# Kernel tuning notes

Hardware: AMD Instinct MI355X
Metric: run time of the kernel (lower is better)

Reference implementation:

```python
import jax, jax.numpy as jnp
import numpy as np

EPROJS = 512
ODIM = 600
DLAYERS = 2
DUNITS = 512
EMBED_DIM = 512
JOINT_DIM = 512
BLANK = 0


def setup_inputs() -> dict:
    key = jax.random.key(0)
    ks = jax.random.split(key, 20)
    B, T, U = 16, 200, 64
    s_d = 1.0 / np.sqrt(DUNITS)
    s_e = 1.0 / np.sqrt(EPROJS)
    s_j = 1.0 / np.sqrt(JOINT_DIM)
    inp = {
        "hs_pad": jax.random.normal(ks[0], (B, T, EPROJS), dtype=jnp.float32),
        "ys_in_pad": jax.random.randint(ks[1], (B, U), 0, ODIM),
        "embed_table": jax.random.normal(ks[2], (ODIM, EMBED_DIM), dtype=jnp.float32).at[BLANK].set(0.0),
        # LSTMCell layer 0: input EMBED_DIM -> DUNITS (gates i,f,g,o stacked => 4*DUNITS)
        "W_ih0": jax.random.uniform(ks[3], (4 * DUNITS, EMBED_DIM), minval=-s_d, maxval=s_d),
        "W_hh0": jax.random.uniform(ks[4], (4 * DUNITS, DUNITS), minval=-s_d, maxval=s_d),
        "b_ih0": jax.random.uniform(ks[5], (4 * DUNITS,), minval=-s_d, maxval=s_d),
        "b_hh0": jax.random.uniform(ks[6], (4 * DUNITS,), minval=-s_d, maxval=s_d),
        # LSTMCell layer 1: DUNITS -> DUNITS
        "W_ih1": jax.random.uniform(ks[7], (4 * DUNITS, DUNITS), minval=-s_d, maxval=s_d),
        "W_hh1": jax.random.uniform(ks[8], (4 * DUNITS, DUNITS), minval=-s_d, maxval=s_d),
        "b_ih1": jax.random.uniform(ks[9], (4 * DUNITS,), minval=-s_d, maxval=s_d),
        "b_hh1": jax.random.uniform(ks[10], (4 * DUNITS,), minval=-s_d, maxval=s_d),
        # joint network
        "W_enc": jax.random.uniform(ks[11], (JOINT_DIM, EPROJS), minval=-s_e, maxval=s_e),
        "b_enc": jax.random.uniform(ks[12], (JOINT_DIM,), minval=-s_e, maxval=s_e),
        "W_dec": jax.random.uniform(ks[13], (JOINT_DIM, DUNITS), minval=-s_d, maxval=s_d),
        "W_out": jax.random.uniform(ks[14], (ODIM, JOINT_DIM), minval=-s_j, maxval=s_j),
        "b_out": jax.random.uniform(ks[15], (ODIM,), minval=-s_j, maxval=s_j),
    }
    return inp


def _lstm_cell(x, h, c, W_ih, W_hh, b_ih, b_hh):
    gates = x @ W_ih.T + b_ih + h @ W_hh.T + b_hh  # (B, 4*D)
    i, f, g, o = jnp.split(gates, 4, axis=-1)
    c_new = jax.nn.sigmoid(f) * c + jax.nn.sigmoid(i) * jnp.tanh(g)
    h_new = jax.nn.sigmoid(o) * jnp.tanh(c_new)
    return h_new, c_new


def _decode(eys, W_ih0, W_hh0, b_ih0, b_hh0, W_ih1, W_hh1, b_ih1, b_hh1):
    # eys: (B, U, E). Sequential 2-layer LSTM over U via scan.
    B = eys.shape[0]
    z = jnp.zeros((B, DUNITS), dtype=eys.dtype)
    carry0 = (z, z, z, z)  # h0, c0, h1, c1

    def step(carry, ey):
        h0, c0, h1, c1 = carry
        h0, c0 = _lstm_cell(ey, h0, c0, W_ih0, W_hh0, b_ih0, b_hh0)
        h1, c1 = _lstm_cell(h0, h1, c1, W_ih1, W_hh1, b_ih1, b_hh1)
        return (h0, c0, h1, c1), h1

    _, h_dec = jax.lax.scan(step, carry0, jnp.swapaxes(eys, 0, 1))  # (U, B, D)
    return jnp.swapaxes(h_dec, 0, 1)  # (B, U, D)


def reference(hs_pad, ys_in_pad, embed_table, W_ih0, W_hh0, b_ih0, b_hh0,
              W_ih1, W_hh1, b_ih1, b_hh1, W_enc, b_enc, W_dec, W_out, b_out):
    eys = embed_table[ys_in_pad]  # (B, U, E); dropout = identity at p=0
    h_dec = _decode(eys, W_ih0, W_hh0, b_ih0, b_hh0, W_ih1, W_hh1, b_ih1, b_hh1)
    # Joint: project BEFORE broadcasting (thin GEMMs), then broadcast-add.
    enc_p = hs_pad @ W_enc.T + b_enc            # (B, T, J)
    dec_p = h_dec @ W_dec.T                     # (B, U, J)
    z = jnp.tanh(enc_p[:, :, None, :] + dec_p[:, None, :, :])  # (B, T, U, J)
    return z @ W_out.T + b_out                  # (B, T, U, odim)
```

## Files before the change

kernel.cpp:

```cpp
#include <hip/hip_runtime.h>
#include <hip/hip_bf16.h>
#include <stdint.h>

#define DEVI __device__ __forceinline__

typedef unsigned short u16;
typedef __attribute__((ext_vector_type(8))) short short8;
typedef __attribute__((ext_vector_type(4))) float f32x4;
typedef __attribute__((ext_vector_type(16))) float f32x16;

DEVI u16 f2bf(float f) {
  union { float f; uint32_t u; } v; v.f = f;
  return (u16)((v.u + 0x7fffu + ((v.u >> 16) & 1u)) >> 16);
}
DEVI float tanh_c(float x) {
  float e = __expf(x + x);
  float r = __builtin_amdgcn_rcpf(e + 1.0f);
  return __builtin_fmaf(-2.0f, r, 1.0f);
}
DEVI float sigm(float x) { return __builtin_amdgcn_rcpf(1.0f + __expf(-x)); }
DEVI uint32_t tj2(float a, float b) {
  float ea = __expf(a + a), eb = __expf(b + b);
  float ta = __builtin_fmaf(-2.0f, __builtin_amdgcn_rcpf(ea + 1.0f), 1.0f);
  float tb = __builtin_fmaf(-2.0f, __builtin_amdgcn_rcpf(eb + 1.0f), 1.0f);
  union { __hip_bfloat162 h; uint32_t u; } cv;
  cv.h = __float22bfloat162_rn(make_float2(ta, tb));
  return cv.u;
}
DEVI short8 ald16(const u16* p) {
  union { unsigned long long q[2]; short8 v; } u;
  u.q[0] = __hip_atomic_load((unsigned long long*)p,       __ATOMIC_RELAXED, __HIP_MEMORY_SCOPE_AGENT);
  u.q[1] = __hip_atomic_load((unsigned long long*)(p + 4), __ATOMIC_RELAXED, __HIP_MEMORY_SCOPE_AGENT);
  return u.v;
}

__global__ void prep_kernel(
    const float* __restrict__ W_ih0, const float* __restrict__ W_hh0,
    const float* __restrict__ W_ih1, const float* __restrict__ W_hh1,
    const float* __restrict__ W_enc, const float* __restrict__ W_dec,
    const float* __restrict__ W_out, const float* __restrict__ embed,
    const float* __restrict__ hs_pad,
    const float* __restrict__ b_ih0, const float* __restrict__ b_hh0,
    const float* __restrict__ b_ih1, const float* __restrict__ b_hh1,
    const float* __restrict__ b_out,
    u16* __restrict__ Wih0b, u16* __restrict__ Whh0b,
    u16* __restrict__ Wih1b, u16* __restrict__ Whh1b,
    u16* __restrict__ Wencb, u16* __restrict__ Wdecb,
    u16* __restrict__ embedb, u16* __restrict__ hsb,
    u16* __restrict__ Wshufb,
    float* __restrict__ bsum0, float* __restrict__ bsum1, float* __restrict__ boutp)
{
  const int c1 = 1048576, c2 = 2097152, c3 = 3145728, c4 = 4194304;
  const int c5 = 4456448, c6 = 4718592, c7 = 5025792, c8 = 6664192;
  const int c9 = 6991872, c10 = 6993920, c11 = 6995968, c12 = 6996608;
  for (int i = blockIdx.x * blockDim.x + threadIdx.x; i < c12; i += gridDim.x * blockDim.x) {
    if (i < c1)       Wih0b[i]      = f2bf(W_ih0[i]);
    else if (i < c2)  Whh0b[i - c1] = f2bf(W_hh0[i - c1]);
    else if (i < c3)  Wih1b[i - c2] = f2bf(W_ih1[i - c2]);
    else if (i < c4)  Whh1b[i - c3] = f2bf(W_hh1[i - c3]);
    else if (i < c5)  Wencb[i - c4] = f2bf(W_enc[i - c4]);
    else if (i < c6)  Wdecb[i - c5] = f2bf(W_dec[i - c5]);
    else if (i < c7)  embedb[i - c6] = f2bf(embed[i - c6]);
    else if (i < c8)  hsb[i - c7]   = f2bf(hs_pad[i - c7]);
    else if (i < c9) {
      int e = i - c8;
      int kc = e / 10240, r = e % 10240;
      int tile = r >> 9, r2 = r & 511;
      int lane = r2 >> 3, ii = r2 & 7;
      int n = tile * 32 + (lane & 31);
      int k = kc * 16 + ((lane >> 5) << 3) + ii;
      Wshufb[e] = (n < 600) ? f2bf(W_out[n * 512 + k]) : (u16)0;
    }
    else if (i < c10) { int n = i - c9;  bsum0[n] = b_ih0[n] + b_hh0[n]; }
    else if (i < c11) { int n = i - c10; bsum1[n] = b_ih1[n] + b_hh1[n]; }
    else              { int n = i - c11; boutp[n] = (n < 600) ? b_out[n] : 0.0f; }
  }
}

template<int MODE, bool AAT, bool SAT>
DEVI void gemm_tile(const u16* __restrict__ A, const u16* __restrict__ B,
                    const int* __restrict__ ys, const float* __restrict__ bias,
                    float* __restrict__ out, int N, int m0, int n0, int tid)
{
  int wv = tid >> 6, l = tid & 63;
  int row = m0 + wv * 16 + (l & 15);
  const u16* arow;
  if (MODE == 1) { int uu = row >> 4, bb = row & 15; arow = A + (size_t)ys[bb * 64 + uu] * 512; }
  else           arow = A + (size_t)row * 512;
  int kof = (l >> 4) * 8;
  arow += kof;
  const u16* br = B + (size_t)(n0 + (l & 15)) * 512 + kof;
  f32x4 a0 = {0.f,0.f,0.f,0.f}, a1 = a0, a2 = a0, a3 = a0;
  for (int kk = 0; kk < 512; kk += 32) {
    short8 av = AAT ? ald16(arow + kk) : *(const short8*)(arow + kk);
    short8 b0 = *(const short8*)(br + kk);
    short8 b1 = *(const short8*)(br + 8192 + kk);
    short8 b2 = *(const short8*)(br + 16384 + kk);
    short8 b3 = *(const short8*)(br + 24576 + kk);
    a0 = __builtin_amdgcn_mfma_f32_16x16x32_bf16(av, b0, a0, 0, 0, 0);
    a1 = __builtin_amdgcn_mfma_f32_16x16x32_bf16(av, b1, a1, 0, 0, 0);
    a2 = __builtin_amdgcn_mfma_f32_16x16x32_bf16(av, b2, a2, 0, 0, 0);
    a3 = __builtin_amdgcn_mfma_f32_16x16x32_bf16(av, b3, a3, 0, 0, 0);
  }
  int col = l & 15, rb = m0 + wv * 16 + (l >> 4) * 4;
  f32x4 accs[4] = {a0, a1, a2, a3};
#pragma unroll
  for (int g = 0; g < 4; ++g) {
    int n = n0 + g * 16 + col;
    float bs = bias ? bias[n] : 0.0f;
#pragma unroll
    for (int i2 = 0; i2 < 4; ++i2) {
      float v = accs[g][i2] + bs;
      if (SAT)
        __hip_atomic_store(&out[(size_t)(rb + i2) * N + n], v,
                           __ATOMIC_RELAXED, __HIP_MEMORY_SCOPE_AGENT);
      else
        out[(size_t)(rb + i2) * N + n] = v;
    }
  }
}

#define L0WG 32
#define FUSED_WG 1136

DEVI void waitflags(const int* f0, const int* f1, const int* xc, int n0, int n1, int xneed) {
  if (threadIdx.x < 64) {
    int l = threadIdx.x;
    for (;;) {
      int a = __hip_atomic_load((int*)(f0 + (l & 31) * 16), __ATOMIC_RELAXED, __HIP_MEMORY_SCOPE_AGENT);
      int b = __hip_atomic_load((int*)(f1 + l * 16),        __ATOMIC_RELAXED, __HIP_MEMORY_SCOPE_AGENT);
      int c = xc ? __hip_atomic_load((int*)xc, __ATOMIC_RELAXED, __HIP_MEMORY_SCOPE_AGENT) : xneed;
      if (__all(a >= n0 && b >= n1 && c >= xneed)) break;
      __builtin_amdgcn_s_sleep(1);
    }
    __builtin_amdgcn_fence(__ATOMIC_ACQUIRE, "agent");
  }
  __syncthreads();
}
DEVI void postflag(int* slot, int val) {
  __syncthreads();
  if (threadIdx.x == 0)
    __hip_atomic_store(slot, val, __ATOMIC_RELAXED, __HIP_MEMORY_SCOPE_AGENT);
}
DEVI const u16* haddr(const u16* base, int slot, int k, int b) {
  return base + slot * 8192 + (k >> 4) * 256 + b * 16 + (k & 15);
}
DEVI void hstore(u16* base, int idx, u16 mine, int tid) {
  int other = __shfl_xor((int)mine, 1);
  if (!(tid & 1)) {
    uint32_t pkv = (uint32_t)mine | (((uint32_t)other & 0xffffu) << 16);
    __hip_atomic_store((uint32_t*)(base + idx), pkv, __ATOMIC_RELAXED, __HIP_MEMORY_SCOPE_AGENT);
  }
}

__global__ __launch_bounds__(256) void lstm_fused(
    const u16* __restrict__ embedb, const u16* __restrict__ Wih0b,
    const int* __restrict__ ys, const float* __restrict__ bsum0,
    float* __restrict__ Xg0,
    const u16* __restrict__ hsb, const u16* __restrict__ Wencb,
    const float* __restrict__ b_enc, float* __restrict__ enc_p,
    const u16* __restrict__ Wdecb, float* __restrict__ dec_p,
    const u16* __restrict__ Whh0, const u16* __restrict__ Wih1, const u16* __restrict__ Whh1,
    const float* __restrict__ bsum1,
    u16* __restrict__ h0b, u16* __restrict__ h1b,
    u16* __restrict__ Hdec,
    int* __restrict__ flags0, int* __restrict__ flags1, int* __restrict__ xcnt)
{
  __shared__ float red[16][256];
  const int bid = blockIdx.x, tid = threadIdx.x;
  const int wv = tid >> 6, l = tid & 63;
  const int lb = l & 15, kof = (l >> 4) * 8;
  const int drb = (l >> 4) * 4;

  if (bid >= 96) {
    if (bid < 608) {
      int g = bid - 96, mt = g >> 5, nt = g & 31;
      gemm_tile<1, false, true>(embedb, Wih0b, ys, bsum0, Xg0, 2048,
                                mt * 64, nt * 64, tid);
      asm volatile("s_waitcnt vmcnt(0)" ::: "memory");
      __syncthreads();
      if (tid == 0)
        __hip_atomic_fetch_add(xcnt + mt, 1, __ATOMIC_RELAXED, __HIP_MEMORY_SCOPE_AGENT);
    } else if (bid < 1008) {
      int g = bid - 608, mt = g >> 3, nt = g & 7;
      gemm_tile<0, false, false>(hsb, Wencb, nullptr, b_enc, enc_p, 512,
                                 mt * 64, nt * 64, tid);
    } else {
      int g = bid - 1008, mt = g >> 3, nt = g & 7;
      const int need = mt * 4 + 4;
      if (tid < 64) {
        for (;;) {
          int a = __hip_atomic_load((int*)(flags1 + tid * 16), __ATOMIC_RELAXED, __HIP_MEMORY_SCOPE_AGENT);
          if (__all(a >= need)) break;
          __builtin_amdgcn_s_sleep(8);
        }
        __builtin_amdgcn_fence(__ATOMIC_ACQUIRE, "agent");
      }
      __syncthreads();
      gemm_tile<0, true, false>(Hdec, Wdecb, nullptr, nullptr, dec_p, 512,
                                mt * 64, nt * 64, tid);
    }
    return;
  }

  if (bid < L0WG) {
    const int be = tid >> 4, je = tid & 15, jg = (bid << 4) + je;
    short8 breg[16];
#pragma unroll
    for (int g = 0; g < 4; ++g) {
      const u16* bp = Whh0 + (size_t)(g * 512 + bid * 16 + lb) * 512 + wv * 128 + kof;
#pragma unroll
      for (int ks = 0; ks < 4; ++ks)
        breg[g * 4 + ks] = *(const short8*)(bp + ks * 32);
    }
    float c0 = 0.f;
    for (int t = 0; t < 64; ++t) {
      waitflags(flags0, flags1, xcnt + (t >> 2), t, (t > 7) ? (t - 7) : 0, 32);
      const float* xg = Xg0 + (size_t)((t << 4) + be) * 2048 + jg;
      float x0 = __hip_atomic_load((float*)(xg),        __ATOMIC_RELAXED, __HIP_MEMORY_SCOPE_AGENT);
      float x1 = __hip_atomic_load((float*)(xg + 512),  __ATOMIC_RELAXED, __HIP_MEMORY_SCOPE_AGENT);
      float x2 = __hip_atomic_load((float*)(xg + 1024), __ATOMIC_RELAXED, __HIP_MEMORY_SCOPE_AGENT);
      float x3 = __hip_atomic_load((float*)(xg + 1536), __ATOMIC_RELAXED, __HIP_MEMORY_SCOPE_AGENT);
      const int rs = (t + 7) & 7;
      f32x4 g0 = {0.f,0.f,0.f,0.f}, g1 = g0, g2 = g0, g3 = g0;
#pragma unroll
      for (int ks = 0; ks < 4; ++ks) {
        int kk = wv * 128 + ks * 32 + kof;
        short8 av = ald16(haddr(h0b, rs, kk, lb));
        g0 = __builtin_amdgcn_mfma_f32_16x16x32_bf16(av, breg[0 * 4 + ks], g0, 0, 0, 0);
        g1 = __builtin_amdgcn_mfma_f32_16x16x32_bf16(av, breg[1 * 4 + ks], g1, 0, 0, 0);
        g2 = __builtin_amdgcn_mfma_f32_16x16x32_bf16(av, breg[2 * 4 + ks], g2, 0, 0, 0);
        g3 = __builtin_amdgcn_mfma_f32_16x16x32_bf16(av, breg[3 * 4 + ks], g3, 0, 0, 0);
      }
      f32x4 gs[4] = {g0, g1, g2, g3};
#pragma unroll
      for (int g = 0; g < 4; ++g)
#pragma unroll
        for (int i2 = 0; i2 < 4; ++i2)
          red[wv * 4 + g][(drb + i2) * 16 + lb] = gs[g][i2];
      __syncthreads();
      {
        float s0 = 0, s1 = 0, s2 = 0, s3 = 0;
#pragma unroll
        for (int v2 = 0; v2 < 4; ++v2) {
          s0 += red[v2 * 4 + 0][be * 16 + je]; s1 += red[v2 * 4 + 1][be * 16 + je];
          s2 += red[v2 * 4 + 2][be * 16 + je]; s3 += red[v2 * 4 + 3][be * 16 + je];
        }
        float gi = s0 + x0, gf = s1 + x1, gg = s2 + x2, go = s3 + x3;
        float I = sigm(gi), F = sigm(gf), G = tanh_c(gg), O = sigm(go);
        c0 = F * c0 + I * G;
        float h0 = O * tanh_c(c0);
        hstore(h0b, ((t & 7) * 32 + bid) * 256 + (tid & ~1), f2bf(h0), tid);
      }
      postflag(flags0 + bid * 16, t + 1);
    }
  } else {
    const int v = bid - L0WG;
    const u16* base0 = (wv < 2) ? Wih1 : Whh1;
    const int kbase = (wv & 1) * 256;
    short8 breg[16];
#pragma unroll
    for (int tt = 0; tt < 2; ++tt) {
      int c = tt * 16 + lb, gate = c >> 3, du = c & 7;
      const u16* bp = base0 + (size_t)(gate * 512 + v * 8 + du) * 512 + kbase + kof;
#pragma unroll
      for (int ks = 0; ks < 8; ++ks)
        breg[tt * 8 + ks] = *(const short8*)(bp + ks * 32);
    }
    float bs0 = 0, bs1 = 0, bs2 = 0, bs3 = 0, c1 = 0.f;
    if (tid < 128) {
      int du = tid & 7, ju = v * 8 + du;
      bs0 = bsum1[ju]; bs1 = bsum1[512 + ju]; bs2 = bsum1[1024 + ju]; bs3 = bsum1[1536 + ju];
    }
    for (int t = 0; t < 64; ++t) {
      waitflags(flags0, flags1, nullptr, t + 1, t, 0);
      const u16* hsrc = (wv < 2) ? (h0b + (t & 7) * 8192) : (h1b + ((t + 7) & 7) * 8192);
      f32x4 g0 = {0.f,0.f,0.f,0.f}, g1 = g0;
#pragma unroll
      for (int ks = 0; ks < 8; ++ks) {
        int kk = kbase + ks * 32 + kof;
        short8 av = ald16(hsrc + (kk >> 4) * 256 + lb * 16 + (kk & 15));
        g0 = __builtin_amdgcn_mfma_f32_16x16x32_bf16(av, breg[0 * 8 + ks], g0, 0, 0, 0);
        g1 = __builtin_amdgcn_mfma_f32_16x16x32_bf16(av, breg[1 * 8 + ks], g1, 0, 0, 0);
      }
#pragma unroll
      for (int i2 = 0; i2 < 4; ++i2) {
        red[wv * 2 + 0][(drb + i2) * 16 + lb] = g0[i2];
        red[wv * 2 + 1][(drb + i2) * 16 + lb] = g1[i2];
      }
      __syncthreads();
      if (tid < 128) {
        int be = tid >> 3, du = tid & 7, ju = v * 8 + du;
        float sg[4] = {bs0, bs1, bs2, bs3};
#pragma unroll
        for (int g = 0; g < 4; ++g) {
          int c = g * 8 + du, tt = c >> 4, cc = c & 15;
          float acc = 0.f;
#pragma unroll
          for (int w2 = 0; w2 < 4; ++w2) acc += red[w2 * 2 + tt][be * 16 + cc];
          sg[g] += acc;
        }
        float I = sigm(sg[0]), F = sigm(sg[1]), G = tanh_c(sg[2]), O = sigm(sg[3]);
        c1 = F * c1 + I * G;
        float h1v = O * tanh_c(c1);
        u16 hb = f2bf(h1v);
        int idx = ((t & 7) * 32 + (ju >> 4)) * 256 + be * 16 + (ju & 15);
        hstore(h1b, idx & ~1, hb, tid);
        hstore(Hdec, ((t << 4) + be) * 512 + (ju & ~1), hb, tid);
      }
      postflag(flags1 + v * 16, t + 1);
    }
  }
}

__global__ __launch_bounds__(256) void joint_kernel(
    const float* __restrict__ enc_p,
    const float* __restrict__ dec_p,
    const u16* __restrict__ Wshuf,
    const float* __restrict__ boutp,
    float* __restrict__ out)
{
  __shared__ int4 wlds[2][1280];
  __shared__ int4 zlds[2][256];
  int bid = blockIdx.x;
  int b = bid / 400, rem = bid % 400;
  int tb = rem / 8, rem2 = rem % 8;
  int ub = rem2 >> 1, nh = rem2 & 1;
  int tid = threadIdx.x, wv = tid >> 6, l = tid & 63;
  int mv = wv >> 1, nv = wv & 1;
  int ln31 = l & 31, lh = l >> 5;
  const int tile0 = nv * 5;
  f32x16 acc[5];
#pragma unroll
  for (int j = 0; j < 5; ++j) {
    float bv = boutp[nh * 320 + (tile0 + j) * 32 + ln31];
#pragma unroll
    for (int g = 0; g < 16; ++g) acc[j][g] = bv;
  }
  int zr = tid & 63, zg = tid >> 6;
  const float* er = enc_p + (size_t)(b * 200 + tb * 4 + (zr >> 4)) * 512 + zg * 8;
  const float* dr = dec_p + (size_t)((ub * 16 + (zr & 15)) * 16 + b) * 512 + zg * 8;
  const int zslot = ((zg >> 1) * 2 + (zr >> 5)) * 64 + ((zg & 1) << 5) + (zr & 31);
  const int4* gW = (const int4*)Wshuf;
  const int nhof = nh * 640;
  const int L0 = tid, L1 = 256 + tid, L2 = 512 + tid + ((tid >= 128) ? 640 : 0),
            L3 = 1408 + tid, L4 = 1664 + tid;
  const int S2 = 512 + tid;

  int4 aw0, aw1, aw2, aw3, aw4; float4 ae0, ae1, ad0, ad1;
  int4 bw0, bw1, bw2, bw3, bw4; float4 be0, be1, bd0, bd1;

  {
    int4 w0 = gW[nhof + L0], w1 = gW[nhof + L1], w2 = gW[nhof + L2],
         w3 = gW[nhof + L3], w4 = gW[nhof + L4];
    float4 e0 = *(const float4*)(er),     e1 = *(const float4*)(er + 4);
    float4 d0 = *(const float4*)(dr),     d1 = *(const float4*)(dr + 4);
    const int cb1 = 2560 + nhof;
    aw0 = gW[cb1 + L0]; aw1 = gW[cb1 + L1]; aw2 = gW[cb1 + L2];
    aw3 = gW[cb1 + L3]; aw4 = gW[cb1 + L4];
    ae0 = *(const float4*)(er + 32); ae1 = *(const float4*)(er + 36);
    ad0 = *(const float4*)(dr + 32); ad1 = *(const float4*)(dr + 36);
    int4 pk;
    pk.x = (int)tj2(e0.x + d0.x, e0.y + d0.y);
    pk.y = (int)tj2(e0.z + d0.z, e0.w + d0.w);
    pk.z = (int)tj2(e1.x + d1.x, e1.y + d1.y);
    pk.w = (int)tj2(e1.z + d1.z, e1.w + d1.w);
    zlds[0][zslot] = pk;
    wlds[0][tid] = w0; wlds[0][256 + tid] = w1; wlds[0][S2] = w2;
    wlds[0][768 + tid] = w3; wlds[0][1024 + tid] = w4;
    __syncthreads();
  }

#define JBODY(C, CUR, NXT, W0, W1, W2, W3, W4, E0, E1, D0, D1,                  \
              PW0, PW1, PW2, PW3, PW4, PE0, PE1, PD0, PD1)                      \
  {                                                                             \
    if ((C) + 2 <= 15) {                                                        \
      const int cb = ((C) + 2) * 2560 + nhof;                                   \
      PW0 = gW[cb + L0]; PW1 = gW[cb + L1]; PW2 = gW[cb + L2];                  \
      PW3 = gW[cb + L3]; PW4 = gW[cb + L4];                                     \
      int k0 = ((C) + 2) * 32;                                                  \
      PE0 = *(const float4*)(er + k0); PE1 = *(const float4*)(er + k0 + 4);     \
      PD0 = *(const float4*)(dr + k0); PD1 = *(const float4*)(dr + k0 + 4);     \
    }                                                                           \
    _Pragma("unroll")                                                           \
    for (int ks = 0; ks < 2; ++ks) {                                            \
      short8 aA = *(const short8*)&zlds[CUR][(ks * 2 + mv) * 64 + l];           \
      _Pragma("unroll")                                                         \
      for (int j = 0; j < 5; ++j) {                                             \
        short8 bw = *(const short8*)&wlds[CUR][ks * 640 + (tile0 + j) * 64 + l];\
        acc[j] = __builtin_amdgcn_mfma_f32_32x32x16_bf16(aA, bw, acc[j], 0, 0, 0); \
      }                                                                         \
    }                                                                           \
    if ((C) + 1 <= 15) {                                                        \
      wlds[NXT][tid] = W0; wlds[NXT][256 + tid] = W1; wlds[NXT][S2] = W2;       \
      wlds[NXT][768 + tid] = W3; wlds[NXT][1024 + tid] = W4;                    \
      int4 pk;                                                                  \
      pk.x = (int)tj2(E0.x + D0.x, E0.y + D0.y);                                \
      pk.y = (int)tj2(E0.z + D0.z, E0.w + D0.w);                                \
      pk.z = (int)tj2(E1.x + D1.x, E1.y + D1.y);                                \
      pk.w = (int)tj2(E1.z + D1.z, E1.w + D1.w);                                \
      zlds[NXT][zslot] = pk;                                                    \
    }                                                                           \
    __syncthreads();                                                            \
  }

  for (int cc = 0; cc < 8; ++cc) {
    const int c0 = cc * 2;
    JBODY(c0,     0, 1, aw0, aw1, aw2, aw3, aw4, ae0, ae1, ad0, ad1,
                        bw0, bw1, bw2, bw3, bw4, be0, be1, bd0, bd1);
    JBODY(c0 + 1, 1, 0, bw0, bw1, bw2, bw3, bw4, be0, be1, bd0, bd1,
                        aw0, aw1, aw2, aw3, aw4, ae0, ae1, ad0, ad1);
  }
#undef JBODY

#pragma unroll
  for (int j = 0; j < 5; ++j) {
    int n = nh * 320 + (tile0 + j) * 32 + ln31;
    if (n < 600) {
      int rbase = mv * 32 + 4 * lh;
#pragma unroll
      for (int g = 0; g < 16; ++g) {
        int r = rbase + (g & 3) + ((g >> 2) << 3);
        int tt = tb * 4 + (r >> 4), uu = ub * 16 + (r & 15);
        __builtin_nontemporal_store(
            acc[j][g], &out[(size_t)((b * 200 + tt) * 64 + uu) * 600 + n]);
      }
    }
  }
}

extern "C" void kernel_launch(void* const* d_in, const int* in_sizes, int n_in,
                              void* d_out, int out_size, void* d_ws, size_t ws_size,
                              hipStream_t stream) {
  const float* hs_pad = (const float*)d_in[0];
  const int*   ys     = (const int*)d_in[1];
  const float* embed  = (const float*)d_in[2];
  const float* W_ih0  = (const float*)d_in[3];
  const float* W_hh0  = (const float*)d_in[4];
  const float* b_ih0  = (const float*)d_in[5];
  const float* b_hh0  = (const float*)d_in[6];
  const float* W_ih1  = (const float*)d_in[7];
  const float* W_hh1  = (const float*)d_in[8];
  const float* b_ih1  = (const float*)d_in[9];
  const float* b_hh1  = (const float*)d_in[10];
  const float* W_enc  = (const float*)d_in[11];
  const float* b_enc  = (const float*)d_in[12];
  const float* W_dec  = (const float*)d_in[13];
  const float* W_out  = (const float*)d_in[14];
  const float* b_out  = (const float*)d_in[15];
  float* out = (float*)d_out;

  uint8_t* ws = (uint8_t*)d_ws;
  size_t off = 0;
  auto alloc = [&](size_t bytes) -> void* {
    void* p = ws + off;
    off = (off + bytes + 255) & ~(size_t)255;
    return p;
  };
  int* flags0   = (int*)alloc(2048);
  int* flags1   = (int*)alloc(4096);
  int* xcnt     = (int*)alloc(256);
  u16* h0buf    = (u16*)alloc(8 * 32 * 256 * 2);
  u16* h1buf    = (u16*)alloc(8 * 32 * 256 * 2);
  u16* Hdec     = (u16*)alloc(64 * 16 * 512 * 2);
  float* Xg0    = (float*)alloc(1024 * 2048 * 4);
  float* enc_p  = (float*)alloc(3200 * 512 * 4);
  float* dec_p  = (float*)alloc(1024 * 512 * 4);
  u16* Wih0b    = (u16*)alloc(2048 * 512 * 2);
  u16* Whh0b    = (u16*)alloc(2048 * 512 * 2);
  u16* Wih1b    = (u16*)alloc(2048 * 512 * 2);
  u16* Whh1b    = (u16*)alloc(2048 * 512 * 2);
  u16* Wencb    = (u16*)alloc(512 * 512 * 2);
  u16* Wdecb    = (u16*)alloc(512 * 512 * 2);
  u16* embedb   = (u16*)alloc(600 * 512 * 2);
  u16* hsb      = (u16*)alloc(3200 * 512 * 2);
  u16* Wshufb   = (u16*)alloc(32 * 20 * 64 * 8 * 2);
  float* bsum0  = (float*)alloc(2048 * 4);
  float* bsum1  = (float*)alloc(2048 * 4);
  float* boutp  = (float*)alloc(640 * 4);

  (void)hipMemsetAsync(d_ws, 0, 2048 + 4096 + 256 + 131072 + 131072, stream);

  prep_kernel<<<2048, 256, 0, stream>>>(
      W_ih0, W_hh0, W_ih1, W_hh1, W_enc, W_dec, W_out, embed, hs_pad,
      b_ih0, b_hh0, b_ih1, b_hh1, b_out,
      Wih0b, Whh0b, Wih1b, Whh1b, Wencb, Wdecb, embedb, hsb, Wshufb,
      bsum0, bsum1, boutp);

  lstm_fused<<<FUSED_WG, 256, 0, stream>>>(
      embedb, Wih0b, ys, bsum0, Xg0,
      hsb, Wencb, b_enc, enc_p,
      Wdecb, dec_p,
      Whh0b, Wih1b, Whh1b, bsum1,
      h0buf, h1buf, Hdec, flags0, flags1, xcnt);

  joint_kernel<<<6400, 256, 0, stream>>>(enc_p, dec_p, Wshufb, boutp, out);
}
```

Before: 625.0 us.

## Fuse joint network into LSTM kernel with per-U-block readiness counters

Moves the Xg0 and enc_p GEMMs into a separate preceding kernel and merges the LSTM recurrence, dec_p projection and joint network into one persistent kernel. Joint blocks spin on per-U-block counters of finished dec_p tiles, so joint work for early time steps can overlap the sequential LSTM tail instead of waiting for a kernel boundary. This removes the xcnt dependency wait inside the recurrence at the cost of an extra launch. It relies on the LSTM blocks being scheduled before the spinning joint blocks, which risks deadlock or wasted CU occupancy from spinning blocks.

```diff
diff --git a/kernel.cpp b/kernel.cpp
--- a/kernel.cpp
+++ b/kernel.cpp
@@ -31,6 +31,12 @@
   union { unsigned long long q[2]; short8 v; } u;
   u.q[0] = __hip_atomic_load((unsigned long long*)p,       __ATOMIC_RELAXED, __HIP_MEMORY_SCOPE_AGENT);
   u.q[1] = __hip_atomic_load((unsigned long long*)(p + 4), __ATOMIC_RELAXED, __HIP_MEMORY_SCOPE_AGENT);
+  return u.v;
+}
+DEVI float4 aldf4(const float* p) {
+  union { unsigned long long q[2]; float4 v; } u;
+  u.q[0] = __hip_atomic_load((unsigned long long*)p,       __ATOMIC_RELAXED, __HIP_MEMORY_SCOPE_AGENT);
+  u.q[1] = __hip_atomic_load((unsigned long long*)(p + 2), __ATOMIC_RELAXED, __HIP_MEMORY_SCOPE_AGENT);
   return u.v;
 }
 
@@ -120,17 +126,35 @@
   }
 }
 
+__global__ __launch_bounds__(256) void gemm_pre(
+    const u16* __restrict__ embedb, const u16* __restrict__ Wih0b,
+    const int* __restrict__ ys, const float* __restrict__ bsum0,
+    float* __restrict__ Xg0,
+    const u16* __restrict__ hsb, const u16* __restrict__ Wencb,
+    const float* __restrict__ b_enc, float* __restrict__ enc_p)
+{
+  int bid = blockIdx.x, tid = threadIdx.x;
+  if (bid < 512) {
+    int mt = bid >> 5, nt = bid & 31;
+    gemm_tile<1, false, false>(embedb, Wih0b, ys, bsum0, Xg0, 2048,
+                               mt * 64, nt * 64, tid);
+  } else {
+    int g = bid - 512, mt = g >> 3, nt = g & 7;
+    gemm_tile<0, false, false>(hsb, Wencb, nullptr, b_enc, enc_p, 512,
+                               mt * 64, nt * 64, tid);
+  }
+}
+
 #define L0WG 32
-#define FUSED_WG 1136
-
-DEVI void waitflags(const int* f0, const int* f1, const int* xc, int n0, int n1, int xneed) {
+#define MEGA_WG 6624
+
+DEVI void waitflags(const int* f0, const int* f1, int n0, int n1) {
   if (threadIdx.x < 64) {
     int l = threadIdx.x;
     for (;;) {
       int a = __hip_atomic_load((int*)(f0 + (l & 31) * 16), __ATOMIC_RELAXED, __HIP_MEMORY_SCOPE_AGENT);
       int b = __hip_atomic_load((int*)(f1 + l * 16),        __ATOMIC_RELAXED, __HIP_MEMORY_SCOPE_AGENT);
-      int c = xc ? __hip_atomic_load((int*)xc, __ATOMIC_RELAXED, __HIP_MEMORY_SCOPE_AGENT) : xneed;
-      if (__all(a >= n0 && b >= n1 && c >= xneed)) break;
+      if (__all(a >= n0 && b >= n1)) break;
       __builtin_amdgcn_s_sleep(1);
     }
     __builtin_amdgcn_fence(__ATOMIC_ACQUIRE, "agent");
@@ -139,8 +163,10 @@
 }
 DEVI void postflag(int* slot, int val) {
   __syncthreads();
-  if (threadIdx.x == 0)
+  if (threadIdx.x == 0) {
+    asm volatile("s_waitcnt vmcnt(0)" ::: "memory");
     __hip_atomic_store(slot, val, __ATOMIC_RELAXED, __HIP_MEMORY_SCOPE_AGENT);
+  }
 }
 DEVI const u16* haddr(const u16* base, int slot, int k, int b) {
   return base + slot * 8192 + (k >> 4) * 256 + b * 16 + (k & 15);
@@ -153,223 +179,81 @@
   }
 }
 
-__global__ __launch_bounds__(256) void lstm_fused(
-    const u16* __restrict__ embedb, const u16* __restrict__ Wih0b,
-    const int* __restrict__ ys, const float* __restrict__ bsum0,
-    float* __restrict__ Xg0,
-    const u16* __restrict__ hsb, const u16* __restrict__ Wencb,
-    const float* __restrict__ b_enc, float* __restrict__ enc_p,
-    const u16* __restrict__ Wdecb, float* __restrict__ dec_p,
+__global__ __launch_bounds__(256) void mega_kernel(
+    const float* __restrict__ Xg0,
     const u16* __restrict__ Whh0, const u16* __restrict__ Wih1, const u16* __restrict__ Whh1,
     const float* __restrict__ bsum1,
     u16* __restrict__ h0b, u16* __restrict__ h1b,
     u16* __restrict__ Hdec,
-    int* __restrict__ flags0, int* __restrict__ flags1, int* __restrict__ xcnt)
+    const u16* __restrict__ Wdecb, float* __restrict__ dec_p,
+    const float* __restrict__ enc_p, const u16* __restrict__ Wshuf,
+    const float* __restrict__ boutp, float* __restrict__ out,
+    int* __restrict__ flags0, int* __restrict__ flags1, int* __restrict__ dcnt)
 {
-  __shared__ float red[16][256];
+  __shared__ int4 smem[3072];
   const int bid = blockIdx.x, tid = threadIdx.x;
   const int wv = tid >> 6, l = tid & 63;
-  const int lb = l & 15, kof = (l >> 4) * 8;
-  const int drb = (l >> 4) * 4;
-
-  if (bid >= 96) {
-    if (bid < 608) {
-      int g = bid - 96, mt = g >> 5, nt = g & 31;
-      gemm_tile<1, false, true>(embedb, Wih0b, ys, bsum0, Xg0, 2048,
-                                mt * 64, nt * 64, tid);
-      asm volatile("s_waitcnt vmcnt(0)" ::: "memory");
+
+  if (bid >= 224) {
+    int jbid = bid - 224;
+    int ub = jbid / 1600, rem = jbid % 1600;
+    int b = rem / 100, r2 = rem % 100;
+    int tb = r2 >> 1, nh = r2 & 1;
+    if (tid == 0) {
+      for (;;) {
+        int c = __hip_atomic_load(dcnt + ub * 16, __ATOMIC_RELAXED, __HIP_MEMORY_SCOPE_AGENT);
+        if (c >= 32) break;
+        __builtin_amdgcn_s_sleep(32);
+      }
+      __builtin_amdgcn_fence(__ATOMIC_ACQUIRE, "agent");
+    }
+    __syncthreads();
+
+    int4 (*wlds)[1280] = (int4(*)[1280])smem;
+    int4 (*zlds)[256]  = (int4(*)[256])(smem + 2560);
+    int mv = wv >> 1, nv = wv & 1;
+    int ln31 = l & 31, lh = l >> 5;
+    const int tile0 = nv * 5;
+    f32x16 acc[5];
+#pragma unroll
+    for (int j = 0; j < 5; ++j) {
+      float bv = boutp[nh * 320 + (tile0 + j) * 32 + ln31];
+#pragma unroll
+      for (int g = 0; g < 16; ++g) acc[j][g] = bv;
+    }
+    int zr = tid & 63, zg = tid >> 6;
+    const float* er = enc_p + (size_t)(b * 200 + tb * 4 + (zr >> 4)) * 512 + zg * 8;
+    const float* dr = dec_p + (size_t)((ub * 16 + (zr & 15)) * 16 + b) * 512 + zg * 8;
+    const int zslot = ((zg >> 1) * 2 + (zr >> 5)) * 64 + ((zg & 1) << 5) + (zr & 31);
+    const int4* gW = (const int4*)Wshuf;
+    const int nhof = nh * 640;
+    const int L0 = tid, L1 = 256 + tid, L2 = 512 + tid + ((tid >= 128) ? 640 : 0),
+              L3 = 1408 + tid, L4 = 1664 + tid;
+    const int S2 = 512 + tid;
+
+    int4 aw0, aw1, aw2, aw3, aw4; float4 ae0, ae1, ad0, ad1;
+    int4 bw0, bw1, bw2, bw3, bw4; float4 be0, be1, bd0, bd1;
+
+    {
+      int4 w0 = gW[nhof + L0], w1 = gW[nhof + L1], w2 = gW[nhof + L2],
+           w3 = gW[nhof + L3], w4 = gW[nhof + L4];
+      float4 e0 = *(const float4*)(er),  e1 = *(const float4*)(er + 4);
+      float4 d0 = aldf4(dr),             d1 = aldf4(dr + 4);
+      const int cb1 = 2560 + nhof;
+      aw0 = gW[cb1 + L0]; aw1 = gW[cb1 + L1]; aw2 = gW[cb1 + L2];
+      aw3 = gW[cb1 + L3]; aw4 = gW[cb1 + L4];
+      ae0 = *(const float4*)(er + 32); ae1 = *(const float4*)(er + 36);
+      ad0 = aldf4(dr + 32);            ad1 = aldf4(dr + 36);
+      int4 pk;
+      pk.x = (int)tj2(e0.x + d0.x, e0.y + d0.y);
+      pk.y = (int)tj2(e0.z + d0.z, e0.w + d0.w);
+      pk.z = (int)tj2(e1.x + d1.x, e1.y + d1.y);
+      pk.w = (int)tj2(e1.z + d1.z, e1.w + d1.w);
+      zlds[0][zslot] = pk;
+      wlds[0][tid] = w0; wlds[0][256 + tid] = w1; wlds[0][S2] = w2;
+      wlds[0][768 + tid] = w3; wlds[0][1024 + tid] = w4;
       __syncthreads();
-      if (tid == 0)
-        __hip_atomic_fetch_add(xcnt + mt, 1, __ATOMIC_RELAXED, __HIP_MEMORY_SCOPE_AGENT);
-    } else if (bid < 1008) {
-      int g = bid - 608, mt = g >> 3, nt = g & 7;
-      gemm_tile<0, false, false>(hsb, Wencb, nullptr, b_enc, enc_p, 512,
-                                 mt * 64, nt * 64, tid);
-    } else {
-      int g = bid - 1008, mt = g >> 3, nt = g & 7;
-      const int need = mt * 4 + 4;
-      if (tid < 64) {
-        for (;;) {
-          int a = __hip_atomic_load((int*)(flags1 + tid * 16), __ATOMIC_RELAXED, __HIP_MEMORY_SCOPE_AGENT);
-          if (__all(a >= need)) break;
-          __builtin_amdgcn_s_sleep(8);
-        }
-        __builtin_amdgcn_fence(__ATOMIC_ACQUIRE, "agent");
-      }
-      __syncthreads();
-      gemm_tile<0, true, false>(Hdec, Wdecb, nullptr, nullptr, dec_p, 512,
-                                mt * 64, nt * 64, tid);
-    }
-    return;
-  }
-
-  if (bid < L0WG) {
-    const int be = tid >> 4, je = tid & 15, jg = (bid << 4) + je;
-    short8 breg[16];
-#pragma unroll
-    for (int g = 0; g < 4; ++g) {
-      const u16* bp = Whh0 + (size_t)(g * 512 + bid * 16 + lb) * 512 + wv * 128 + kof;
-#pragma unroll
-      for (int ks = 0; ks < 4; ++ks)
-        breg[g * 4 + ks] = *(const short8*)(bp + ks * 32);
-    }
-    float c0 = 0.f;
-    for (int t = 0; t < 64; ++t) {
-      waitflags(flags0, flags1, xcnt + (t >> 2), t, (t > 7) ? (t - 7) : 0, 32);
-      const float* xg = Xg0 + (size_t)((t << 4) + be) * 2048 + jg;
-      float x0 = __hip_atomic_load((float*)(xg),        __ATOMIC_RELAXED, __HIP_MEMORY_SCOPE_AGENT);
-      float x1 = __hip_atomic_load((float*)(xg + 512),  __ATOMIC_RELAXED, __HIP_MEMORY_SCOPE_AGENT);
-      float x2 = __hip_atomic_load((float*)(xg + 1024), __ATOMIC_RELAXED, __HIP_MEMORY_SCOPE_AGENT);
-      float x3 = __hip_atomic_load((float*)(xg + 1536), __ATOMIC_RELAXED, __HIP_MEMORY_SCOPE_AGENT);
-      const int rs = (t + 7) & 7;
-      f32x4 g0 = {0.f,0.f,0.f,0.f}, g1 = g0, g2 = g0, g3 = g0;
-#pragma unroll
-      for (int ks = 0; ks < 4; ++ks) {
-        int kk = wv * 128 + ks * 32 + kof;
-        short8 av = ald16(haddr(h0b, rs, kk, lb));
-        g0 = __builtin_amdgcn_mfma_f32_16x16x32_bf16(av, breg[0 * 4 + ks], g0, 0, 0, 0);
-        g1 = __builtin_amdgcn_mfma_f32_16x16x32_bf16(av, breg[1 * 4 + ks], g1, 0, 0, 0);
-        g2 = __builtin_amdgcn_mfma_f32_16x16x32_bf16(av, breg[2 * 4 + ks], g2, 0, 0, 0);
-        g3 = __builtin_amdgcn_mfma_f32_16x16x32_bf16(av, breg[3 * 4 + ks], g3, 0, 0, 0);
-      }
-      f32x4 gs[4] = {g0, g1, g2, g3};
-#pragma unroll
-      for (int g = 0; g < 4; ++g)
-#pragma unroll
-        for (int i2 = 0; i2 < 4; ++i2)
-          red[wv * 4 + g][(drb + i2) * 16 + lb] = gs[g][i2];
-      __syncthreads();
-      {
-        float s0 = 0, s1 = 0, s2 = 0, s3 = 0;
-#pragma unroll
-        for (int v2 = 0; v2 < 4; ++v2) {
-          s0 += red[v2 * 4 + 0][be * 16 + je]; s1 += red[v2 * 4 + 1][be * 16 + je];
-          s2 += red[v2 * 4 + 2][be * 16 + je]; s3 += red[v2 * 4 + 3][be * 16 + je];
-        }
-        float gi = s0 + x0, gf = s1 + x1, gg = s2 + x2, go = s3 + x3;
-        float I = sigm(gi), F = sigm(gf), G = tanh_c(gg), O = sigm(go);
-        c0 = F * c0 + I * G;
-        float h0 = O * tanh_c(c0);
-        hstore(h0b, ((t & 7) * 32 + bid) * 256 + (tid & ~1), f2bf(h0), tid);
-      }
-      postflag(flags0 + bid * 16, t + 1);
-    }
-  } else {
-    const int v = bid - L0WG;
-    const u16* base0 = (wv < 2) ? Wih1 : Whh1;
-    const int kbase = (wv & 1) * 256;
-    short8 breg[16];
-#pragma unroll
-    for (int tt = 0; tt < 2; ++tt) {
-      int c = tt * 16 + lb, gate = c >> 3, du = c & 7;
-      const u16* bp = base0 + (size_t)(gate * 512 + v * 8 + du) * 512 + kbase + kof;
-#pragma unroll
-      for (int ks = 0; ks < 8; ++ks)
-        breg[tt * 8 + ks] = *(const short8*)(bp + ks * 32);
-    }
-    float bs0 = 0, bs1 = 0, bs2 = 0, bs3 = 0, c1 = 0.f;
-    if (tid < 128) {
-      int du = tid & 7, ju = v * 8 + du;
-      bs0 = bsum1[ju]; bs1 = bsum1[512 + ju]; bs2 = bsum1[1024 + ju]; bs3 = bsum1[1536 + ju];
-    }
-    for (int t = 0; t < 64; ++t) {
-      waitflags(flags0, flags1, nullptr, t + 1, t, 0);
-      const u16* hsrc = (wv < 2) ? (h0b + (t & 7) * 8192) : (h1b + ((t + 7) & 7) * 8192);
-      f32x4 g0 = {0.f,0.f,0.f,0.f}, g1 = g0;
-#pragma unroll
-      for (int ks = 0; ks < 8; ++ks) {
-        int kk = kbase + ks * 32 + kof;
-        short8 av = ald16(hsrc + (kk >> 4) * 256 + lb * 16 + (kk & 15));
-        g0 = __builtin_amdgcn_mfma_f32_16x16x32_bf16(av, breg[0 * 8 + ks], g0, 0, 0, 0);
-        g1 = __builtin_amdgcn_mfma_f32_16x16x32_bf16(av, breg[1 * 8 + ks], g1, 0, 0, 0);
-      }
-#pragma unroll
-      for (int i2 = 0; i2 < 4; ++i2) {
-        red[wv * 2 + 0][(drb + i2) * 16 + lb] = g0[i2];
-        red[wv * 2 + 1][(drb + i2) * 16 + lb] = g1[i2];
-      }
-      __syncthreads();
-      if (tid < 128) {
-        int be = tid >> 3, du = tid & 7, ju = v * 8 + du;
-        float sg[4] = {bs0, bs1, bs2, bs3};
-#pragma unroll
-        for (int g = 0; g < 4; ++g) {
-          int c = g * 8 + du, tt = c >> 4, cc = c & 15;
-          float acc = 0.f;
-#pragma unroll
-          for (int w2 = 0; w2 < 4; ++w2) acc += red[w2 * 2 + tt][be * 16 + cc];
-          sg[g] += acc;
-        }
-        float I = sigm(sg[0]), F = sigm(sg[1]), G = tanh_c(sg[2]), O = sigm(sg[3]);
-        c1 = F * c1 + I * G;
-        float h1v = O * tanh_c(c1);
-        u16 hb = f2bf(h1v);
-        int idx = ((t & 7) * 32 + (ju >> 4)) * 256 + be * 16 + (ju & 15);
-        hstore(h1b, idx & ~1, hb, tid);
-        hstore(Hdec, ((t << 4) + be) * 512 + (ju & ~1), hb, tid);
-      }
-      postflag(flags1 + v * 16, t + 1);
-    }
-  }
-}
-
-__global__ __launch_bounds__(256) void joint_kernel(
-    const float* __restrict__ enc_p,
-    const float* __restrict__ dec_p,
-    const u16* __restrict__ Wshuf,
-    const float* __restrict__ boutp,
-    float* __restrict__ out)
-{
-  __shared__ int4 wlds[2][1280];
-  __shared__ int4 zlds[2][256];
-  int bid = blockIdx.x;
-  int b = bid / 400, rem = bid % 400;
-  int tb = rem / 8, rem2 = rem % 8;
-  int ub = rem2 >> 1, nh = rem2 & 1;
-  int tid = threadIdx.x, wv = tid >> 6, l = tid & 63;
-  int mv = wv >> 1, nv = wv & 1;
-  int ln31 = l & 31, lh = l >> 5;
-  const int tile0 = nv * 5;
-  f32x16 acc[5];
-#pragma unroll
-  for (int j = 0; j < 5; ++j) {
-    float bv = boutp[nh * 320 + (tile0 + j) * 32 + ln31];
-#pragma unroll
-    for (int g = 0; g < 16; ++g) acc[j][g] = bv;
-  }
-  int zr = tid & 63, zg = tid >> 6;
-  const float* er = enc_p + (size_t)(b * 200 + tb * 4 + (zr >> 4)) * 512 + zg * 8;
-  const float* dr = dec_p + (size_t)((ub * 16 + (zr & 15)) * 16 + b) * 512 + zg * 8;
-  const int zslot = ((zg >> 1) * 2 + (zr >> 5)) * 64 + ((zg & 1) << 5) + (zr & 31);
-  const int4* gW = (const int4*)Wshuf;
-  const int nhof = nh * 640;
-  const int L0 = tid, L1 = 256 + tid, L2 = 512 + tid + ((tid >= 128) ? 640 : 0),
-            L3 = 1408 + tid, L4 = 1664 + tid;
-  const int S2 = 512 + tid;
-
-  int4 aw0, aw1, aw2, aw3, aw4; float4 ae0, ae1, ad0, ad1;
-  int4 bw0, bw1, bw2, bw3, bw4; float4 be0, be1, bd0, bd1;
-
-  {
-    int4 w0 = gW[nhof + L0], w1 = gW[nhof + L1], w2 = gW[nhof + L2],
-         w3 = gW[nhof + L3], w4 = gW[nhof + L4];
-    float4 e0 = *(const float4*)(er),     e1 = *(const float4*)(er + 4);
-    float4 d0 = *(const float4*)(dr),     d1 = *(const float4*)(dr + 4);
-    const int cb1 = 2560 + nhof;
-    aw0 = gW[cb1 + L0]; aw1 = gW[cb1 + L1]; aw2 = gW[cb1 + L2];
-    aw3 = gW[cb1 + L3]; aw4 = gW[cb1 + L4];
-    ae0 = *(const float4*)(er + 32); ae1 = *(const float4*)(er + 36);
-    ad0 = *(const float4*)(dr + 32); ad1 = *(const float4*)(dr + 36);
-    int4 pk;
-    pk.x = (int)tj2(e0.x + d0.x, e0.y + d0.y);
-    pk.y = (int)tj2(e0.z + d0.z, e0.w + d0.w);
-    pk.z = (int)tj2(e1.x + d1.x, e1.y + d1.y);
-    pk.w = (int)tj2(e1.z + d1.z, e1.w + d1.w);
-    zlds[0][zslot] = pk;
-    wlds[0][tid] = w0; wlds[0][256 + tid] = w1; wlds[0][S2] = w2;
-    wlds[0][768 + tid] = w3; wlds[0][1024 + tid] = w4;
-    __syncthreads();
-  }
+    }
 
 #define JBODY(C, CUR, NXT, W0, W1, W2, W3, W4, E0, E1, D0, D1,                  \
               PW0, PW1, PW2, PW3, PW4, PE0, PE1, PD0, PD1)                      \
@@ -380,7 +264,7 @@
       PW3 = gW[cb + L3]; PW4 = gW[cb + L4];                                     \
       int k0 = ((C) + 2) * 32;                                                  \
       PE0 = *(const float4*)(er + k0); PE1 = *(const float4*)(er + k0 + 4);     \
-      PD0 = *(const float4*)(dr + k0); PD1 = *(const float4*)(dr + k0 + 4);     \
+      PD0 = aldf4(dr + k0);            PD1 = aldf4(dr + k0 + 4);                \
     }                                                                           \
     _Pragma("unroll")                                                           \
     for (int ks = 0; ks < 2; ++ks) {                                            \
@@ -404,27 +288,160 @@
     __syncthreads();                                                            \
   }
 
-  for (int cc = 0; cc < 8; ++cc) {
-    const int c0 = cc * 2;
-    JBODY(c0,     0, 1, aw0, aw1, aw2, aw3, aw4, ae0, ae1, ad0, ad1,
-                        bw0, bw1, bw2, bw3, bw4, be0, be1, bd0, bd1);
-    JBODY(c0 + 1, 1, 0, bw0, bw1, bw2, bw3, bw4, be0, be1, bd0, bd1,
-                        aw0, aw1, aw2, aw3, aw4, ae0, ae1, ad0, ad1);
-  }
+    for (int cc = 0; cc < 8; ++cc) {
+      const int c0 = cc * 2;
+      JBODY(c0,     0, 1, aw0, aw1, aw2, aw3, aw4, ae0, ae1, ad0, ad1,
+                          bw0, bw1, bw2, bw3, bw4, be0, be1, bd0, bd1);
+      JBODY(c0 + 1, 1, 0, bw0, bw1, bw2, bw3, bw4, be0, be1, bd0, bd1,
+                          aw0, aw1, aw2, aw3, aw4, ae0, ae1, ad0, ad1);
+    }
 #undef JBODY
 
 #pragma unroll
-  for (int j = 0; j < 5; ++j) {
-    int n = nh * 320 + (tile0 + j) * 32 + ln31;
-    if (n < 600) {
-      int rbase = mv * 32 + 4 * lh;
-#pragma unroll
-      for (int g = 0; g < 16; ++g) {
-        int r = rbase + (g & 3) + ((g >> 2) << 3);
-        int tt = tb * 4 + (r >> 4), uu = ub * 16 + (r & 15);
-        __builtin_nontemporal_store(
-            acc[j][g], &out[(size_t)((b * 200 + tt) * 64 + uu) * 600 + n]);
-      }
+    for (int j = 0; j < 5; ++j) {
+      int n = nh * 320 + (tile0 + j) * 32 + ln31;
+      if (n < 600) {
+        int rbase = mv * 32 + 4 * lh;
+#pragma unroll
+        for (int g = 0; g < 16; ++g) {
+          int r = rbase + (g & 3) + ((g >> 2) << 3);
+          int tt = tb * 4 + (r >> 4), uu = ub * 16 + (r & 15);
+          __builtin_nontemporal_store(
+              acc[j][g], &out[(size_t)((b * 200 + tt) * 64 + uu) * 600 + n]);
+        }
+      }
+    }
+    return;
+  }
+
+  if (bid >= 96) {
+    int g = bid - 96, mt = g >> 3, nt = g & 7;
+    const int need = mt * 4 + 4;
+    if (tid < 64) {
+      for (;;) {
+        int a = __hip_atomic_load((int*)(flags1 + tid * 16), __ATOMIC_RELAXED, __HIP_MEMORY_SCOPE_AGENT);
+        if (__all(a >= need)) break;
+        __builtin_amdgcn_s_sleep(16);
+      }
+      __builtin_amdgcn_fence(__ATOMIC_ACQUIRE, "agent");
+    }
+    __syncthreads();
+    gemm_tile<0, true, true>(Hdec, Wdecb, nullptr, nullptr, dec_p, 512,
+                             mt * 64, nt * 64, tid);
+    asm volatile("s_waitcnt vmcnt(0)" ::: "memory");
+    __syncthreads();
+    if (tid == 0)
+      __hip_atomic_fetch_add(dcnt + (mt >> 2) * 16, 1, __ATOMIC_RELAXED, __HIP_MEMORY_SCOPE_AGENT);
+    return;
+  }
+
+  float (*red)[256] = (float(*)[256])smem;
+  const int lb = l & 15, kof = (l >> 4) * 8;
+  const int drb = (l >> 4) * 4;
+
+  if (bid < L0WG) {
+    const int be = tid >> 4, je = tid & 15, jg = (bid << 4) + je;
+    short8 breg[16];
+#pragma unroll
+    for (int g = 0; g < 4; ++g) {
+      const u16* bp = Whh0 + (size_t)(g * 512 + bid * 16 + lb) * 512 + wv * 128 + kof;
+#pragma unroll
+      for (int ks = 0; ks < 4; ++ks)
+        breg[g * 4 + ks] = *(const short8*)(bp + ks * 32);
+    }
+    float c0 = 0.f;
+    for (int t = 0; t < 64; ++t) {
+      const float* xg = Xg0 + (size_t)((t << 4) + be) * 2048 + jg;
+      float x0 = xg[0], x1 = xg[512], x2 = xg[1024], x3 = xg[1536];
+      waitflags(flags0, flags1, t, (t > 7) ? (t - 7) : 0);
+      const int rs = (t + 7) & 7;
+      f32x4 g0 = {0.f,0.f,0.f,0.f}, g1 = g0, g2 = g0, g3 = g0;
+#pragma unroll
+      for (int ks = 0; ks < 4; ++ks) {
+        int kk = wv * 128 + ks * 32 + kof;
+        short8 av = ald16(haddr(h0b, rs, kk, lb));
+        g0 = __builtin_amdgcn_mfma_f32_16x16x32_bf16(av, breg[0 * 4 + ks], g0, 0, 0, 0);
+        g1 = __builtin_amdgcn_mfma_f32_16x16x32_bf16(av, breg[1 * 4 + ks], g1, 0, 0, 0);
+        g2 = __builtin_amdgcn_mfma_f32_16x16x32_bf16(av, breg[2 * 4 + ks], g2, 0, 0, 0);
+        g3 = __builtin_amdgcn_mfma_f32_16x16x32_bf16(av, breg[3 * 4 + ks], g3, 0, 0, 0);
+      }
+      f32x4 gs[4] = {g0, g1, g2, g3};
+#pragma unroll
+      for (int g = 0; g < 4; ++g)
+#pragma unroll
+        for (int i2 = 0; i2 < 4; ++i2)
+          red[wv * 4 + g][(drb + i2) * 16 + lb] = gs[g][i2];
+      __syncthreads();
+      {
+        float s0 = 0, s1 = 0, s2 = 0, s3 = 0;
+#pragma unroll
+        for (int v2 = 0; v2 < 4; ++v2) {
+          s0 += red[v2 * 4 + 0][be * 16 + je]; s1 += red[v2 * 4 + 1][be * 16 + je];
+          s2 += red[v2 * 4 + 2][be * 16 + je]; s3 += red[v2 * 4 + 3][be * 16 + je];
+        }
+        float gi = s0 + x0, gf = s1 + x1, gg = s2 + x2, go = s3 + x3;
+        float I = sigm(gi), F = sigm(gf), G = tanh_c(gg), O = sigm(go);
+        c0 = F * c0 + I * G;
+        float h0 = O * tanh_c(c0);
+        hstore(h0b, ((t & 7) * 32 + bid) * 256 + (tid & ~1), f2bf(h0), tid);
+      }
+      postflag(flags0 + bid * 16, t + 1);
+    }
+  } else {
+    const int v = bid - L0WG;
+    const u16* base0 = (wv < 2) ? Wih1 : Whh1;
+    const int kbase = (wv & 1) * 256;
+    short8 breg[16];
+#pragma unroll
+    for (int tt = 0; tt < 2; ++tt) {
+      int c = tt * 16 + lb, gate = c >> 3, du = c & 7;
+      const u16* bp = base0 + (size_t)(gate * 512 + v * 8 + du) * 512 + kbase + kof;
+#pragma unroll
+      for (int ks = 0; ks < 8; ++ks)
+        breg[tt * 8 + ks] = *(const short8*)(bp + ks * 32);
+    }
+    float bs0 = 0, bs1 = 0, bs2 = 0, bs3 = 0, c1 = 0.f;
+    if (tid < 128) {
+      int du = tid & 7, ju = v * 8 + du;
+      bs0 = bsum1[ju]; bs1 = bsum1[512 + ju]; bs2 = bsum1[1024 + ju]; bs3 = bsum1[1536 + ju];
+    }
+    for (int t = 0; t < 64; ++t) {
+      waitflags(flags0, flags1, t + 1, t);
+      const u16* hsrc = (wv < 2) ? (h0b + (t & 7) * 8192) : (h1b + ((t + 7) & 7) * 8192);
+      f32x4 g0 = {0.f,0.f,0.f,0.f}, g1 = g0;
+#pragma unroll
+      for (int ks = 0; ks < 8; ++ks) {
+        int kk = kbase + ks * 32 + kof;
+        short8 av = ald16(hsrc + (kk >> 4) * 256 + lb * 16 + (kk & 15));
+        g0 = __builtin_amdgcn_mfma_f32_16x16x32_bf16(av, breg[0 * 8 + ks], g0, 0, 0, 0);
+        g1 = __builtin_amdgcn_mfma_f32_16x16x32_bf16(av, breg[1 * 8 + ks], g1, 0, 0, 0);
+      }
+#pragma unroll
+      for (int i2 = 0; i2 < 4; ++i2) {
+        red[wv * 2 + 0][(drb + i2) * 16 + lb] = g0[i2];
+        red[wv * 2 + 1][(drb + i2) * 16 + lb] = g1[i2];
+      }
+      __syncthreads();
+      if (tid < 128) {
+        int be = tid >> 3, du = tid & 7, ju = v * 8 + du;
+        float sg[4] = {bs0, bs1, bs2, bs3};
+#pragma unroll
+        for (int g = 0; g < 4; ++g) {
+          int c = g * 8 + du, tt = c >> 4, cc = c & 15;
+          float acc = 0.f;
+#pragma unroll
+          for (int w2 = 0; w2 < 4; ++w2) acc += red[w2 * 2 + tt][be * 16 + cc];
+          sg[g] += acc;
+        }
+        float I = sigm(sg[0]), F = sigm(sg[1]), G = tanh_c(sg[2]), O = sigm(sg[3]);
+        c1 = F * c1 + I * G;
+        float h1v = O * tanh_c(c1);
+        u16 hb = f2bf(h1v);
+        int idx = ((t & 7) * 32 + (ju >> 4)) * 256 + be * 16 + (ju & 15);
+        hstore(h1b, idx & ~1, hb, tid);
+        hstore(Hdec, ((t << 4) + be) * 512 + (ju & ~1), hb, tid);
+      }
+      postflag(flags1 + v * 16, t + 1);
     }
   }
 }
@@ -459,7 +476,7 @@
   };
   int* flags0   = (int*)alloc(2048);
   int* flags1   = (int*)alloc(4096);
-  int* xcnt     = (int*)alloc(256);
+  int* dcnt     = (int*)alloc(256);
   u16* h0buf    = (u16*)alloc(8 * 32 * 256 * 2);
   u16* h1buf    = (u16*)alloc(8 * 32 * 256 * 2);
   u16* Hdec     = (u16*)alloc(64 * 16 * 512 * 2);
@@ -487,12 +504,12 @@
       Wih0b, Whh0b, Wih1b, Whh1b, Wencb, Wdecb, embedb, hsb, Wshufb,
       bsum0, bsum1, boutp);
 
-  lstm_fused<<<FUSED_WG, 256, 0, stream>>>(
-      embedb, Wih0b, ys, bsum0, Xg0,
-      hsb, Wencb, b_enc, enc_p,
-      Wdecb, dec_p,
-      Whh0b, Wih1b, Whh1b, bsum1,
-      h0buf, h1buf, Hdec, flags0, flags1, xcnt);
-
-  joint_kernel<<<6400, 256, 0, stream>>>(enc_p, dec_p, Wshufb, boutp, out);
-}
+  gemm_pre<<<912, 256, 0, stream>>>(embedb, Wih0b, ys, bsum0, Xg0,
+                                    hsb, Wencb, b_enc, enc_p);
+
+  mega_kernel<<<MEGA_WG, 256, 0, stream>>>(
+      Xg0, Whh0b, Wih1b, Whh1b, bsum1,
+      h0buf, h1buf, Hdec, Wdecb, dec_p,
+      enc_p, Wshufb, boutp, out,
+      flags0, flags1, dcnt);
+}
```

Measured after the change: 614.0 us. About the same (-1.8%).
